# Performance work log

Hardware: AMD Instinct MI355X
Metric: run time of the kernel (lower is better)

## Reference

```python
import jax, jax.numpy as jnp
import numpy as np

DEPTH_DIM = 256
SAMPLE_RANGE = (-6.0, 6.0)
LOG_SQRT_2PI = 0.5 * np.log(2.0 * np.pi).astype(np.float32)


def _d_coors():
    # cat(linspace(lo, 0, D), linspace(0, hi, D)) -> length 2*D
    d1 = jnp.linspace(SAMPLE_RANGE[0], 0.0, DEPTH_DIM, dtype=jnp.float32)
    d2 = jnp.linspace(0.0, SAMPLE_RANGE[1], DEPTH_DIM, dtype=jnp.float32)
    return jnp.concatenate([d1, d2])  # [2*D]


def setup_inputs() -> dict:
    key = jax.random.key(0)
    k1, k2, k3, k4 = jax.random.split(key, 4)
    pts_num, H, W = 200000, 256, 704
    u = jax.random.randint(k1, (pts_num, 1), 0, W, dtype=jnp.int32)
    v = jax.random.randint(k2, (pts_num, 1), 0, H, dtype=jnp.int32)
    pts_pos = jnp.concatenate([u, v], axis=1)                      # [N,2] (x=u, y=v)
    pts_depth = jax.random.randint(k3, (pts_num, 1), 0, DEPTH_DIM, dtype=jnp.int32)
    pts_conf = jax.random.uniform(k4, (pts_num, 1), jnp.float32, 0.5, 3.0)  # Normal scale > 0
    return {"pts_pos": pts_pos, "pts_depth": pts_depth, "pts_conf": pts_conf,
            "feat_h": H, "feat_w": W}


def reference(pts_pos, pts_depth, pts_conf, feat_h, feat_w):
    d_coors = _d_coors()
    # Analytic window: boolean-mask gather == contiguous slice starting at D-1-depth
    start = (DEPTH_DIM - 1) - pts_depth                              # [N,1]
    idx = start + jnp.arange(DEPTH_DIM, dtype=jnp.int32)[None, :]    # [N,D]
    x = d_coors[idx]                                                 # [N,D]
    # Normal(0, sigma).log_prob -> pdf
    z = x / pts_conf
    logp = -0.5 * z * z - jnp.log(pts_conf) - LOG_SQRT_2PI
    probs = jnp.exp(logp)                                            # [N,D]
    # F.normalize(p=2, dim=-1, eps=1e-12)
    nrm = jnp.sqrt(jnp.sum(probs * probs, axis=-1, keepdims=True))
    probs = probs / jnp.maximum(nrm, 1e-12)
    # scatter-add per-point depth distributions into [D, H, W] map
    lin = pts_pos[:, 1] * feat_w + pts_pos[:, 0]                     # [N]
    flat = jnp.zeros((feat_h * feat_w, DEPTH_DIM), jnp.float32).at[lin].add(probs)
    return flat.reshape(feat_h, feat_w, DEPTH_DIM).transpose(2, 0, 1)
```

## Files before the change

### kernel.cpp

```cpp
#include <hip/hip_runtime.h>

#define D_DIM 256
#define STEP (6.0f / 255.0f)
#define CAP 16
#define LOG2E 1.4426950408889634f

__global__ __launch_bounds__(256) void normfill_kernel(
    const int2* __restrict__ pts_pos, const int* __restrict__ pts_depth,
    const float* __restrict__ pts_conf, const int* __restrict__ feat_w,
    int* __restrict__ counts, float4* __restrict__ bins, int N)
{
    const int p = blockIdx.x * 256 + threadIdx.x;
    if (p >= N) return;

    const int dep = pts_depth[p];
    const float ic = 1.0f / pts_conf[p];
    const float s  = STEP * ic;
    const float s2 = s * s;
    const float a  = -0.5f * s2;

    const float c0 = 0.8862269254527580f / s;
    const float n1 = (float)dep;
    const float n2 = (float)(254 - dep);
    const float E1 = __expf(-s2 * n1 * n1);
    const float E2 = __expf(-s2 * n2 * n2);
    const float F1 = c0 * erff(s * n1) + 0.5f * (1.f + E1) - s2 * n1 * E1 * (1.f / 6.f);
    const float F2 = c0 * erff(s * n2) + 0.5f * (1.f + E2) - s2 * n2 * E2 * (1.f / 6.f);
    const float ss = F1 + F2;

    const int W = *feat_w;
    const int2 uv = pts_pos[p];
    const int lin = uv.y * W + uv.x;
    const int slot = atomicAdd(&counts[lin], 1);
    if (slot < CAP) {
        const float A2 = a * LOG2E;
        float4 rec;
        rec.x = __int_as_float(dep);
        rec.y = A2;
        rec.z = rsqrtf(ss);
        rec.w = exp2f(2.0f * A2);
        bins[(size_t)lin * CAP + slot] = rec;
    }
}

__global__ __launch_bounds__(256) void gather_kernel(
    const int* __restrict__ counts, const float4* __restrict__ bins,
    float* __restrict__ out, int HW)
{
    const int wave = threadIdx.x >> 6;
    const int lane = threadIdx.x & 63;
    const int pix = blockIdx.x * 64 + lane;
    const int db  = blockIdx.y * 128 + wave * 32;

    float acc[32];
#pragma unroll
    for (int k = 0; k < 32; ++k) acc[k] = 0.f;

    if (pix < HW) {
        int cnt = counts[pix];
        cnt = cnt < CAP ? cnt : CAP;
        const float4* __restrict__ rec = bins + (size_t)pix * CAP;
        for (int j = 0; j < cnt; ++j) {
            const float4 r4 = rec[j];
            const int dep   = __float_as_int(r4.x);
            const float A2  = r4.y;
            const float inv = r4.z;
            const float Q   = r4.w;

            const int t0  = db - dep;
            const int xt0 = t0 - (t0 > 0);
            const float fx = (float)xt0;
            float g = exp2f(A2 * fx * fx);
            float r = exp2f(A2 * (2.0f * fx + 1.0f));
            const int skipK = -t0;
#pragma unroll
            for (int k = 0; k < 32; ++k) {
                acc[k] = fmaf(g, inv, acc[k]);
                const bool adv = (k != skipK);
                g = adv ? g * r : g;
                r = adv ? r * Q : r;
            }
        }
    }

    if (pix < HW) {
#pragma unroll
        for (int k = 0; k < 32; ++k) {
            __builtin_nontemporal_store(acc[k], out + (size_t)(db + k) * HW + pix);
        }
    }
}

__global__ __launch_bounds__(256) void scatter_direct_kernel(
    const int* __restrict__ pts_pos, const int* __restrict__ pts_depth,
    const float* __restrict__ pts_conf, const int* __restrict__ feat_w,
    float* __restrict__ out, int HW, int N)
{
    const int wave = threadIdx.x >> 6;
    const int lane = threadIdx.x & 63;
    const int p = blockIdx.x * 4 + wave;
    if (p >= N) return;

    const int W = *feat_w;
    const int lin = pts_pos[2 * p + 1] * W + pts_pos[2 * p];
    const int dep = pts_depth[p];
    const float ic = 1.0f / pts_conf[p];

    float pr[4];
    float ss = 0.f;
#pragma unroll
    for (int k = 0; k < 4; ++k) {
        const int d = lane + 64 * k;
        const int t = d - dep;
        const float x = (float)(t > 0 ? t - 1 : t) * STEP;
        const float z = x * ic;
        const float e = __expf(-0.5f * z * z);
        pr[k] = e;
        ss += e * e;
    }
#pragma unroll
    for (int off = 32; off; off >>= 1) ss += __shfl_xor(ss, off, 64);
    const float inv = rsqrtf(ss);
#pragma unroll
    for (int k = 0; k < 4; ++k) {
        const int d = lane + 64 * k;
        atomicAdd(out + (size_t)d * HW + lin, pr[k] * inv);
    }
}

extern "C" void kernel_launch(void* const* d_in, const int* in_sizes, int n_in,
                              void* d_out, int out_size, void* d_ws, size_t ws_size,
                              hipStream_t stream) {
    const int*   pts_pos   = (const int*)d_in[0];
    const int*   pts_depth = (const int*)d_in[1];
    const float* pts_conf  = (const float*)d_in[2];
    const int*   feat_w    = (const int*)d_in[4];

    const int N  = in_sizes[0] / 2;
    const int HW = out_size / D_DIM;
    float* out = (float*)d_out;

    float4* bins  = (float4*)d_ws;
    int* counts   = (int*)(bins + (size_t)HW * CAP);
    const size_t ws_need = (size_t)HW * CAP * sizeof(float4) + (size_t)HW * sizeof(int);

    if (ws_size >= ws_need) {
        (void)hipMemsetAsync(counts, 0, (size_t)HW * sizeof(int), stream);
        normfill_kernel<<<(N + 255) / 256, 256, 0, stream>>>(
            (const int2*)pts_pos, pts_depth, pts_conf, feat_w, counts, bins, N);
        dim3 grid((HW + 63) / 64, 2);
        gather_kernel<<<grid, 256, 0, stream>>>(counts, bins, out, HW);
    } else {
        (void)hipMemsetAsync(d_out, 0, (size_t)out_size * sizeof(float), stream);
        scatter_direct_kernel<<<(N + 3) / 4, 256, 0, stream>>>(
            pts_pos, pts_depth, pts_conf, feat_w, out, HW, N);
    }
}
```

Baseline: 230.4 us.

## Bin points per 64-pixel tile and accumulate depth profiles in LDS

Points are now binned into 64-pixel tiles with a compact record list of up to 128 per tile, replacing the sparse 16-slot-per-pixel bins. The gather kernel zeroes a 64x256 float tile in shared memory and processes each record with all lanes of a wave. Each lane evaluates the Gaussian directly for one depth and adds it into an XOR-swizzled LDS slot. The tile is then streamed out with nontemporal stores. This is meant to remove per-pixel divergence and the large, sparse workspace reads, but it costs 64KB of LDS per block, which limits occupancy, and it drops points if a tile gets more than 128.

Result: slower. 255.4 us (+10.8%).

```diff
diff --git a/kernel.cpp b/kernel.cpp
--- a/kernel.cpp
+++ b/kernel.cpp
@@ -2,13 +2,13 @@
 
 #define D_DIM 256
 #define STEP (6.0f / 255.0f)
-#define CAP 16
+#define CAP_T 128
 #define LOG2E 1.4426950408889634f
 
 __global__ __launch_bounds__(256) void normfill_kernel(
     const int2* __restrict__ pts_pos, const int* __restrict__ pts_depth,
     const float* __restrict__ pts_conf, const int* __restrict__ feat_w,
-    int* __restrict__ counts, float4* __restrict__ bins, int N)
+    int* __restrict__ counts, float4* __restrict__ recs, int N)
 {
     const int p = blockIdx.x * 256 + threadIdx.x;
     if (p >= N) return;
@@ -17,7 +17,6 @@
     const float ic = 1.0f / pts_conf[p];
     const float s  = STEP * ic;
     const float s2 = s * s;
-    const float a  = -0.5f * s2;
 
     const float c0 = 0.8862269254527580f / s;
     const float n1 = (float)dep;
@@ -31,62 +30,76 @@
     const int W = *feat_w;
     const int2 uv = pts_pos[p];
     const int lin = uv.y * W + uv.x;
-    const int slot = atomicAdd(&counts[lin], 1);
-    if (slot < CAP) {
-        const float A2 = a * LOG2E;
+    const int tileIdx = lin >> 6;
+    const int c = lin & 63;
+    const int slot = atomicAdd(&counts[tileIdx], 1);
+    if (slot < CAP_T) {
         float4 rec;
         rec.x = __int_as_float(dep);
-        rec.y = A2;
+        rec.y = -0.5f * s2 * LOG2E;
         rec.z = rsqrtf(ss);
-        rec.w = exp2f(2.0f * A2);
-        bins[(size_t)lin * CAP + slot] = rec;
+        rec.w = __int_as_float(c);
+        recs[(size_t)tileIdx * CAP_T + slot] = rec;
     }
 }
 
 __global__ __launch_bounds__(256) void gather_kernel(
-    const int* __restrict__ counts, const float4* __restrict__ bins,
+    const int* __restrict__ counts, const float4* __restrict__ recs,
     float* __restrict__ out, int HW)
 {
+    __shared__ float tile[64 * 256];
     const int wave = threadIdx.x >> 6;
     const int lane = threadIdx.x & 63;
-    const int pix = blockIdx.x * 64 + lane;
-    const int db  = blockIdx.y * 128 + wave * 32;
+    const int b = blockIdx.x;
+    const int p0 = b * 64;
+    const int dbase = wave * 64;
 
-    float acc[32];
+    float4* t4 = (float4*)tile;
+    {
+        const int i4 = lane & 15;
+        const int cr = lane >> 4;
 #pragma unroll
-    for (int k = 0; k < 32; ++k) acc[k] = 0.f;
-
-    if (pix < HW) {
-        int cnt = counts[pix];
-        cnt = cnt < CAP ? cnt : CAP;
-        const float4* __restrict__ rec = bins + (size_t)pix * CAP;
-        for (int j = 0; j < cnt; ++j) {
-            const float4 r4 = rec[j];
-            const int dep   = __float_as_int(r4.x);
-            const float A2  = r4.y;
-            const float inv = r4.z;
-            const float Q   = r4.w;
-
-            const int t0  = db - dep;
-            const int xt0 = t0 - (t0 > 0);
-            const float fx = (float)xt0;
-            float g = exp2f(A2 * fx * fx);
-            float r = exp2f(A2 * (2.0f * fx + 1.0f));
-            const int skipK = -t0;
-#pragma unroll
-            for (int k = 0; k < 32; ++k) {
-                acc[k] = fmaf(g, inv, acc[k]);
-                const bool adv = (k != skipK);
-                g = adv ? g * r : g;
-                r = adv ? r * Q : r;
-            }
+        for (int it = 0; it < 16; ++it) {
+            const int c = it * 4 + cr;
+            t4[c * 64 + wave * 16 + i4] = make_float4(0.f, 0.f, 0.f, 0.f);
         }
     }
 
+    int cnt = counts[b];
+    cnt = cnt < CAP_T ? cnt : CAP_T;
+    const float4* __restrict__ rec = recs + (size_t)b * CAP_T;
+
+#define PROC(r)                                                         \
+    {                                                                   \
+        const int dep = __float_as_int((r).x);                          \
+        const int c   = __float_as_int((r).w);                          \
+        const int t   = dbase + lane - dep;                             \
+        const float xt = (float)(t - (t > 0));                          \
+        const float e  = exp2f((r).y * xt * xt) * (r).z;                \
+        tile[c * 256 + dbase + (lane ^ c)] += e;                        \
+    }
+
+    int j = 0;
+    for (; j + 4 <= cnt; j += 4) {
+        const float4 r0 = rec[j];
+        const float4 r1 = rec[j + 1];
+        const float4 r2 = rec[j + 2];
+        const float4 r3 = rec[j + 3];
+        PROC(r0) PROC(r1) PROC(r2) PROC(r3)
+    }
+    for (; j < cnt; ++j) {
+        const float4 r0 = rec[j];
+        PROC(r0)
+    }
+#undef PROC
+
+    const int pix = p0 + lane;
     if (pix < HW) {
 #pragma unroll
-        for (int k = 0; k < 32; ++k) {
-            __builtin_nontemporal_store(acc[k], out + (size_t)(db + k) * HW + pix);
+        for (int rr = 0; rr < 64; ++rr) {
+            const int d = dbase + rr;
+            const float v = tile[lane * 256 + dbase + (rr ^ lane)];
+            __builtin_nontemporal_store(v, out + (size_t)d * HW + pix);
         }
     }
 }
@@ -140,16 +153,16 @@
     const int HW = out_size / D_DIM;
     float* out = (float*)d_out;
 
-    float4* bins  = (float4*)d_ws;
-    int* counts   = (int*)(bins + (size_t)HW * CAP);
-    const size_t ws_need = (size_t)HW * CAP * sizeof(float4) + (size_t)HW * sizeof(int);
+    const int tiles = (HW + 63) / 64;
+    float4* recs = (float4*)d_ws;
+    int* counts  = (int*)(recs + (size_t)tiles * CAP_T);
+    const size_t ws_need = (size_t)tiles * CAP_T * sizeof(float4) + (size_t)tiles * sizeof(int);
 
     if (ws_size >= ws_need) {
-        (void)hipMemsetAsync(counts, 0, (size_t)HW * sizeof(int), stream);
+        (void)hipMemsetAsync(counts, 0, (size_t)tiles * sizeof(int), stream);
         normfill_kernel<<<(N + 255) / 256, 256, 0, stream>>>(
-            (const int2*)pts_pos, pts_depth, pts_conf, feat_w, counts, bins, N);
-        dim3 grid((HW + 63) / 64, 2);
-        gather_kernel<<<grid, 256, 0, stream>>>(counts, bins, out, HW);
+            (const int2*)pts_pos, pts_depth, pts_conf, feat_w, counts, recs, N);
+        gather_kernel<<<tiles, 256, 0, stream>>>(counts, recs, out, HW);
     } else {
         (void)hipMemsetAsync(d_out, 0, (size_t)out_size * sizeof(float), stream);
         scatter_direct_kernel<<<(N + 3) / 4, 256, 0, stream>>>(
```
